# Kernel optimization log

Measured on AMD Instinct MI355X. Metric: run time of the kernel, lower is better.

## Reference

```python
import jax, jax.numpy as jnp
import numpy as np

B, CIN, H, W = 8, 64, 128, 128
COUT, KH, KW = 64, 3, 3
STRIDE, PAD, DIL = 1, 1, 1
HO, WO = 128, 128


def setup_inputs() -> dict:
    key = jax.random.key(0)
    k1, k2, k3 = jax.random.split(key, 3)
    x = jax.random.normal(k1, (B, CIN, H, W), dtype=jnp.float32)
    offset = jax.random.normal(k2, (B, 2 * KH * KW, HO, WO), dtype=jnp.float32)
    fan_in = CIN * KH * KW
    weight = jax.random.normal(k3, (COUT, CIN, KH, KW), dtype=jnp.float32) / np.sqrt(fan_in)
    return {"x": x, "offset": offset, "weight": weight}


def _deform_conv(x, offset, weight):
    b, c, h, w = x.shape
    cout, cin, kh, kw = weight.shape
    k2 = kh * kw
    ho, wo = offset.shape[2], offset.shape[3]
    # offsets: interleaved (dy, dx) per kernel tap
    off = offset.reshape(b, k2, 2, ho, wo)
    dy, dx = off[:, :, 0], off[:, :, 1]                      # [B, K2, Ho, Wo]
    ky = jnp.repeat(jnp.arange(kh), kw).astype(x.dtype)       # [K2]
    kx = jnp.tile(jnp.arange(kw), kh).astype(x.dtype)
    base_y = (jnp.arange(ho) * STRIDE - PAD).astype(x.dtype)  # [Ho]
    base_x = (jnp.arange(wo) * STRIDE - PAD).astype(x.dtype)  # [Wo]
    py = dy + ky[None, :, None, None] * DIL + base_y[None, None, :, None]
    px = dx + kx[None, :, None, None] * DIL + base_x[None, None, None, :]

    y0 = jnp.floor(py)
    x0 = jnp.floor(px)
    wy1 = py - y0
    wx1 = px - x0
    y0i = y0.astype(jnp.int32)
    x0i = x0.astype(jnp.int32)

    def gather_corner(yi, xi, wgt):
        # zero-padding semantics: mask out-of-bounds corners
        valid = ((yi >= 0) & (yi < h) & (xi >= 0) & (xi < w)).astype(x.dtype)
        yc = jnp.clip(yi, 0, h - 1)
        xc = jnp.clip(xi, 0, w - 1)
        def per_batch(xb, yb, xbid, vb, wb):
            return xb[:, yb, xbid] * (vb * wb)[None]          # [C, K2, Ho, Wo]
        return jax.vmap(per_batch)(x, yc, xc, valid, wgt)

    # accumulate 4 corners to avoid holding all gathers at once
    sampled = gather_corner(y0i, x0i, (1 - wy1) * (1 - wx1))
    sampled = sampled + gather_corner(y0i, x0i + 1, (1 - wy1) * wx1)
    sampled = sampled + gather_corner(y0i + 1, x0i, wy1 * (1 - wx1))
    sampled = sampled + gather_corner(y0i + 1, x0i + 1, wy1 * wx1)
    # sampled: [B, Cin, K2, Ho, Wo]; conv-accumulate
    return jnp.einsum('bckhw,ock->bohw', sampled, weight.reshape(cout, cin, k2))


def reference(x, offset, weight):
    return _deform_conv(x, offset, weight)
```

## Files before the change

### kernel.cpp

```cpp
#include <hip/hip_runtime.h>
#include <hip/hip_bf16.h>

#define CIN  64
#define HH   128
#define WW   128
#define COUT 64
#define K2   9
#define HW   (HH * WW)

typedef __attribute__((ext_vector_type(8))) short bf16x8;
typedef __attribute__((ext_vector_type(4))) float f32x4;
typedef __attribute__((ext_vector_type(2))) float f32x2;

__device__ __forceinline__ unsigned short f2bf(float f) {
    __hip_bfloat16 h = __float2bfloat16(f);
    return *reinterpret_cast<unsigned short*>(&h);
}
__device__ __forceinline__ f32x2 up2(unsigned int d) {
    f32x2 r;
    r[0] = __uint_as_float(d << 16);
    r[1] = __uint_as_float(d & 0xffff0000u);
    return r;
}
__device__ __forceinline__ void gl2lds16(const unsigned short* g, unsigned short* l) {
    __builtin_amdgcn_global_load_lds(
        (const __attribute__((address_space(1))) unsigned int*)g,
        (__attribute__((address_space(3))) unsigned int*)l, 16, 0, 0);
}

__launch_bounds__(256)
__global__ void xprep2_kernel(const float* __restrict__ x, unsigned short* __restrict__ xt) {
    const int idx = blockIdx.x * 256 + threadIdx.x;
    const int xw = idx & 127;
    const int y  = (idx >> 7) & 127;
    const int s  = (idx >> 14) & 7;
    const int b  = idx >> 17;
    const float* src = x + (((size_t)(b * CIN + s * 8) * HH) + y) * WW + xw;
    union { unsigned short us[8]; bf16x8 v; } u;
    #pragma unroll
    for (int j = 0; j < 8; ++j) u.us[j] = f2bf(src[(size_t)j * HW]);
    *(bf16x8*)(xt + ((((size_t)b * 8 + s) * HW) + y * WW + xw) * 8) = u.v;
}

__global__ void wprep_kernel(const float* __restrict__ w, unsigned short* __restrict__ wtp) {
    int idx = blockIdx.x * 256 + threadIdx.x;
    if (idx >= COUT * CIN * K2) return;
    int j  = idx & 7;
    int l  = (idx >> 3) & 63;
    int nt = (idx >> 9) & 3;
    int ks = (idx >> 11) & 1;
    int k  = idx >> 12;
    int o  = nt * 16 + (l & 15);
    int c  = ks * 32 + (l >> 4) * 8 + j;
    wtp[idx] = f2bf(w[(o * CIN + c) * K2 + k]);
}

__launch_bounds__(512, 4)
__global__ void dcn_kernel(const unsigned short* __restrict__ xt,
                           const float* __restrict__ off,
                           const unsigned short* __restrict__ wtp,
                           float* __restrict__ out) {
    __shared__ unsigned short lsB[2][4096];
    __shared__ float sred[64][66];

    const int tid = threadIdx.x;
    const int w   = tid >> 6;
    const int l   = tid & 63;
    const int wr  = w & 3;
    const int wh  = w >> 2;

    int bid = blockIdx.x;
    bid = (bid & 7) * 256 + (bid >> 3);
    const int b   = bid >> 8;
    const int t   = bid & 255;
    const int ty0 = (t >> 3) << 2;
    const int tx0 = (t & 7) << 4;

    const int g      = l >> 4;
    const int lane16 = l & 15;

    f32x4 acc[4] = {{0,0,0,0},{0,0,0,0},{0,0,0,0},{0,0,0,0}};

    const float* offb = off + (size_t)b * (2 * K2) * HW;
    const unsigned short* xp = xt + ((size_t)b * 8 + (wh * 4 + g)) * HW * 8;

    const int ypA  = ty0 + wr;
    const int xpA  = tx0 + lane16;
    const int offp = ypA * WW + xpA;

    f32x4 Pw[2];
    int   Pr0[2], Pr1[2];
    float oyv[2], oxv[2];
    bf16x8 Gst[2][4];
    bf16x8 bvv[4];
    bf16x8 af;

#define PARAMS(K, S) do {                                                     \
    const int kdy = (K) / 3 - 1, kdx = (K) % 3 - 1;                           \
    float py = oyv[S] + (float)(ypA + kdy);                                   \
    float px = oxv[S] + (float)(xpA + kdx);                                   \
    float fy = floorf(py), fx = floorf(px);                                   \
    float wy = py - fy, wxn = px - fx;                                        \
    int y0 = (int)fy, x0i = (int)fx;                                          \
    int yc0 = min(max(y0,     0), HH - 1);                                    \
    int yc1 = min(max(y0 + 1, 0), HH - 1);                                    \
    float ay0 = (y0 >= 0  && y0 <= HH - 1) ? (1.f - wy) : 0.f;                \
    float ay1 = (y0 >= -1 && y0 <= HH - 2) ? wy         : 0.f;                \
    int   xL  = min(max(x0i, 0), WW - 2);                                     \
    float bx0 = (x0i >= 0  && x0i <= WW - 1) ? (1.f - wxn) : 0.f;             \
    float bx1 = (x0i >= -1 && x0i <= WW - 2) ? wxn         : 0.f;             \
    bool  sw  = (x0i != xL);                                                  \
    float wxa = sw ? bx1 : bx0;                                               \
    float wxb = sw ? bx0 : bx1;                                               \
    Pw[S][0] = ay0 * wxa; Pw[S][1] = ay0 * wxb;                               \
    Pw[S][2] = ay1 * wxa; Pw[S][3] = ay1 * wxb;                               \
    Pr0[S] = (yc0 * WW + xL) * 8;                                             \
    Pr1[S] = (yc1 * WW + xL) * 8;                                             \
} while (0)

#define GATHER(S) do {                                                        \
    const unsigned short* r0p = xp + Pr0[S];                                  \
    const unsigned short* r1p = xp + Pr1[S];                                  \
    Gst[S][0] = *(const bf16x8*)(r0p); Gst[S][1] = *(const bf16x8*)(r0p + 8); \
    Gst[S][2] = *(const bf16x8*)(r1p); Gst[S][3] = *(const bf16x8*)(r1p + 8); \
} while (0)

#define INTERP(S) do {                                                        \
    union { bf16x8 v; unsigned int d[4]; } ua, ub, uc, ud;                    \
    ua.v = Gst[S][0]; ub.v = Gst[S][1]; uc.v = Gst[S][2]; ud.v = Gst[S][3];   \
    union { unsigned short us[8]; bf16x8 v; } rr;                             \
    _Pragma("unroll")                                                         \
    for (int q = 0; q < 4; ++q) {                                             \
        f32x2 v = up2(ua.d[q]) * Pw[S][0] + up2(ub.d[q]) * Pw[S][1]           \
                + up2(uc.d[q]) * Pw[S][2] + up2(ud.d[q]) * Pw[S][3];          \
        rr.us[2*q]   = f2bf(v[0]);                                            \
        rr.us[2*q+1] = f2bf(v[1]);                                            \
    }                                                                         \
    af = rr.v;                                                                \
} while (0)

#define BVLOAD(P) do {                                                        \
    _Pragma("unroll")                                                         \
    for (int nt = 0; nt < 4; ++nt)                                            \
        bvv[nt] = *(const bf16x8*)(&lsB[P][(wh * 4 + nt) * 512 + l * 8]);     \
} while (0)

#define STAGE(P, K) do {                                                      \
    gl2lds16(wtp + (K) * 4096 + w * 512 + l * 8, &lsB[P][w * 512]);           \
} while (0)

#define DOMFMA() do {                                                         \
    __builtin_amdgcn_s_setprio(1);                                            \
    _Pragma("unroll")                                                         \
    for (int nt = 0; nt < 4; ++nt)                                            \
        acc[nt] = __builtin_amdgcn_mfma_f32_16x16x32_bf16(af, bvv[nt], acc[nt], 0, 0, 0); \
    __builtin_amdgcn_s_setprio(0);                                            \
} while (0)

    STAGE(0, 0);
    oyv[0] = offb[offp];          oxv[0] = offb[HW + offp];
    oyv[1] = offb[2 * HW + offp]; oxv[1] = offb[3 * HW + offp];
    PARAMS(0, 0);
    GATHER(0);
    __syncthreads();

    #pragma unroll
    for (int s = 0; s < K2; ++s) {
        const int cur = s & 1, nxt = cur ^ 1;
        if (s < 8) {
            STAGE(nxt, s + 1);
            PARAMS(s + 1, nxt);
            if (s < 7) {
                oyv[cur] = offb[(2 * (s + 2)    ) * HW + offp];
                oxv[cur] = offb[(2 * (s + 2) + 1) * HW + offp];
            }
            GATHER(nxt);
        }
        BVLOAD(cur);
        INTERP(cur);
        DOMFMA();
        if (s < 8) __syncthreads();
    }

#undef PARAMS
#undef GATHER
#undef INTERP
#undef BVLOAD
#undef STAGE
#undef DOMFMA

    const int rq = g * 4;
    if (wh == 0) {
        #pragma unroll
        for (int nt = 0; nt < 4; ++nt)
            #pragma unroll
            for (int j = 0; j < 4; ++j)
                sred[wr * 16 + rq + j][nt * 16 + lane16] = acc[nt][j];
    }
    __syncthreads();
    if (wh == 1) {
        #pragma unroll
        for (int nt = 0; nt < 4; ++nt) {
            f32x4 v;
            #pragma unroll
            for (int j = 0; j < 4; ++j)
                v[j] = sred[wr * 16 + rq + j][nt * 16 + lane16] + acc[nt][j];
            const int o  = nt * 16 + lane16;
            const int yy = ty0 + wr;
            const int xx = tx0 + rq;
            *(f32x4*)&out[(((size_t)b * COUT + o) * HH + yy) * WW + xx] = v;
        }
    }
}

__global__ void wprep_fb(const float* __restrict__ w, unsigned short* __restrict__ wt) {
    int idx = blockIdx.x * 256 + threadIdx.x;
    if (idx >= COUT * CIN * K2) return;
    int o = idx / (CIN * K2);
    int r = idx % (CIN * K2);
    int k = r / CIN;
    int c = r % CIN;
    wt[idx] = f2bf(w[o * (CIN * K2) + c * K2 + k]);
}

__launch_bounds__(256)
__global__ void dcn_fb(const float* __restrict__ x, const float* __restrict__ off,
                       const unsigned short* __restrict__ wt, float* __restrict__ out) {
    __shared__ unsigned short s_s[64 * 66];
    const int tid = threadIdx.x;
    const int w = tid >> 6, l = tid & 63;
    const int bid = blockIdx.x;
    const int b = bid >> 8, t = bid & 255;
    const int ty0 = (t >> 4) << 3, tx0 = (t & 15) << 3;
    const int iy = l >> 3, ix = l & 7;
    const int ypix = ty0 + iy, xpix = tx0 + ix;
    f32x4 acc[4] = {{0,0,0,0},{0,0,0,0},{0,0,0,0},{0,0,0,0}};
    const int c0w = w * 16;
    for (int k = 0; k < K2; ++k) {
        float dy = off[(((b * (2*K2)) + 2*k    ) * HH + ypix) * WW + xpix];
        float dx = off[(((b * (2*K2)) + 2*k + 1) * HH + ypix) * WW + xpix];
        float py = dy + (float)(k / 3 + ypix - 1);
        float px = dx + (float)(k % 3 + xpix - 1);
        float fy = floorf(py), fx = floorf(px);
        float wy = py - fy, wx = px - fx;
        int y0 = (int)fy, x0 = (int)fx;
        int yc0 = min(max(y0, 0), HH-1), yc1 = min(max(y0+1, 0), HH-1);
        float ay0 = (y0 >= 0 && y0 <= HH-1) ? (1.f-wy) : 0.f;
        float ay1 = (y0 >= -1 && y0 <= HH-2) ? wy : 0.f;
        int xL = min(max(x0, 0), WW-2);
        float bx0 = (x0 >= 0 && x0 <= WW-1) ? (1.f-wx) : 0.f;
        float bx1 = (x0 >= -1 && x0 <= WW-2) ? wx : 0.f;
        bool sw = (x0 != xL);
        float wxa = sw ? bx1 : bx0, wxb = sw ? bx0 : bx1;
        float W0x = ay0*wxa, W0y = ay0*wxb, W1x = ay1*wxa, W1y = ay1*wxb;
        const float* r0 = x + ((b * CIN + c0w) * HH + yc0) * WW + xL;
        const float* r1 = x + ((b * CIN + c0w) * HH + yc1) * WW + xL;
        unsigned short* sd = &s_s[l * 66 + c0w];
        #pragma unroll
        for (int cc = 0; cc < 16; ++cc) {
            sd[cc] = f2bf(W0x*r0[0] + W0y*r0[1] + W1x*r1[0] + W1y*r1[1]);
            r0 += HH*WW; r1 += HH*WW;
        }
        __syncthreads();
        const int o_lane = l & 15, q = l >> 4;
        #pragma unroll
        for (int ks = 0; ks < 2; ++ks) {
            const int cb = ks*32 + q*8;
            const int row = w*16 + o_lane;
            const unsigned int* sp = (const unsigned int*)s_s;
            const int ib = row*33 + (cb >> 1);
            union { unsigned int u[4]; bf16x8 v; } af;
            af.u[0]=sp[ib]; af.u[1]=sp[ib+1]; af.u[2]=sp[ib+2]; af.u[3]=sp[ib+3];
            #pragma unroll
            for (int nt = 0; nt < 4; ++nt) {
                bf16x8 bfv = *(const bf16x8*)(wt + (nt*16 + o_lane) * (CIN*K2) + k*64 + cb);
                acc[nt] = __builtin_amdgcn_mfma_f32_16x16x32_bf16(af.v, bfv, acc[nt], 0, 0, 0);
            }
        }
        __syncthreads();
    }
    const int o_lane = l & 15, rq = (l >> 4) * 4;
    #pragma unroll
    for (int nt = 0; nt < 4; ++nt) {
        const int o = nt*16 + o_lane;
        #pragma unroll
        for (int j = 0; j < 4; ++j) {
            const int pix = w*16 + rq + j;
            out[(((size_t)b * COUT + o) * HH + ty0 + (pix>>3)) * WW + tx0 + (pix&7)] = acc[nt][j];
        }
    }
}

extern "C" void kernel_launch(void* const* d_in, const int* in_sizes, int n_in,
                              void* d_out, int out_size, void* d_ws, size_t ws_size,
                              hipStream_t stream) {
    const float* x   = (const float*)d_in[0];
    const float* off = (const float*)d_in[1];
    const float* wgt = (const float*)d_in[2];
    float* out = (float*)d_out;

    const size_t xt_bytes = (size_t)8 * HW * 64 * sizeof(unsigned short);
    const size_t wt_bytes = (size_t)COUT * CIN * K2 * sizeof(unsigned short);

    if (ws_size >= xt_bytes + wt_bytes) {
        unsigned short* xt  = (unsigned short*)d_ws;
        unsigned short* wtp = (unsigned short*)((char*)d_ws + xt_bytes);
        xprep2_kernel<<<4096, 256, 0, stream>>>(x, xt);
        wprep_kernel<<<(COUT * CIN * K2 + 255) / 256, 256, 0, stream>>>(wgt, wtp);
        dcn_kernel<<<2048, 512, 0, stream>>>(xt, off, wtp, out);
    } else {
        unsigned short* wt = (unsigned short*)d_ws;
        wprep_fb<<<(COUT * CIN * K2 + 255) / 256, 256, 0, stream>>>(wgt, wt);
        dcn_fb<<<2048, 256, 0, stream>>>(x, off, wt, out);
    }
}
```

Measured before the change: 62.20 us.

## Preload all weight taps into LDS once and drop per-tap barriers

Weights for all nine kernel taps are now loaded into dynamic shared memory once at kernel start, replacing the per-tap double-buffered staging. This removes the per-iteration __syncthreads and the interleaved global-to-LDS copies from the main loop. The reduction buffer is aliased onto the same shared memory after a barrier. The cost is a 72 KB LDS footprint per block, which may cut the number of resident blocks per CU and raise the up-front load latency.

Measured after the change: 57.34 us. 7.8% less time.

```diff
diff --git a/kernel.cpp b/kernel.cpp
--- a/kernel.cpp
+++ b/kernel.cpp
@@ -60,9 +60,7 @@
                            const float* __restrict__ off,
                            const unsigned short* __restrict__ wtp,
                            float* __restrict__ out) {
-    __shared__ unsigned short lsB[2][4096];
-    __shared__ float sred[64][66];
-
+    extern __shared__ unsigned short lsB[];
     const int tid = threadIdx.x;
     const int w   = tid >> 6;
     const int l   = tid & 63;
@@ -78,6 +76,12 @@
 
     const int g      = l >> 4;
     const int lane16 = l & 15;
+
+    #pragma unroll
+    for (int r = 0; r < 9; ++r) {
+        const int seg = r * 8 + w;
+        gl2lds16(wtp + seg * 512 + l * 8, lsB + seg * 512);
+    }
 
     f32x4 acc[4] = {{0,0,0,0},{0,0,0,0},{0,0,0,0},{0,0,0,0}};
 
@@ -139,25 +143,21 @@
     af = rr.v;                                                                \
 } while (0)
 
-#define BVLOAD(P) do {                                                        \
+#define BVLOAD(K) do {                                                        \
     _Pragma("unroll")                                                         \
     for (int nt = 0; nt < 4; ++nt)                                            \
-        bvv[nt] = *(const bf16x8*)(&lsB[P][(wh * 4 + nt) * 512 + l * 8]);     \
-} while (0)
-
-#define STAGE(P, K) do {                                                      \
-    gl2lds16(wtp + (K) * 4096 + w * 512 + l * 8, &lsB[P][w * 512]);           \
+        bvv[nt] = *(const bf16x8*)(&lsB[(((K) * 2 + wh) * 4 + nt) * 512 + l * 8]); \
 } while (0)
 
 #define DOMFMA() do {                                                         \
     __builtin_amdgcn_s_setprio(1);                                            \
-    _Pragma("unroll")                                                         \
-    for (int nt = 0; nt < 4; ++nt)                                            \
-        acc[nt] = __builtin_amdgcn_mfma_f32_16x16x32_bf16(af, bvv[nt], acc[nt], 0, 0, 0); \
+    acc[0] = __builtin_amdgcn_mfma_f32_16x16x32_bf16(af, bvv[0], acc[0], 0, 0, 0); \
+    acc[1] = __builtin_amdgcn_mfma_f32_16x16x32_bf16(af, bvv[1], acc[1], 0, 0, 0); \
+    acc[2] = __builtin_amdgcn_mfma_f32_16x16x32_bf16(af, bvv[2], acc[2], 0, 0, 0); \
+    acc[3] = __builtin_amdgcn_mfma_f32_16x16x32_bf16(af, bvv[3], acc[3], 0, 0, 0); \
     __builtin_amdgcn_s_setprio(0);                                            \
 } while (0)
 
-    STAGE(0, 0);
     oyv[0] = offb[offp];          oxv[0] = offb[HW + offp];
     oyv[1] = offb[2 * HW + offp]; oxv[1] = offb[3 * HW + offp];
     PARAMS(0, 0);
@@ -168,7 +168,6 @@
     for (int s = 0; s < K2; ++s) {
         const int cur = s & 1, nxt = cur ^ 1;
         if (s < 8) {
-            STAGE(nxt, s + 1);
             PARAMS(s + 1, nxt);
             if (s < 7) {
                 oyv[cur] = offb[(2 * (s + 2)    ) * HW + offp];
@@ -176,19 +175,19 @@
             }
             GATHER(nxt);
         }
-        BVLOAD(cur);
+        BVLOAD(s);
         INTERP(cur);
         DOMFMA();
-        if (s < 8) __syncthreads();
     }
 
 #undef PARAMS
 #undef GATHER
 #undef INTERP
 #undef BVLOAD
-#undef STAGE
 #undef DOMFMA
 
+    float (*sred)[66] = (float (*)[66])lsB;
+    __syncthreads();
     const int rq = g * 4;
     if (wh == 0) {
         #pragma unroll
@@ -307,7 +306,7 @@
         unsigned short* wtp = (unsigned short*)((char*)d_ws + xt_bytes);
         xprep2_kernel<<<4096, 256, 0, stream>>>(x, xt);
         wprep_kernel<<<(COUT * CIN * K2 + 255) / 256, 256, 0, stream>>>(wgt, wtp);
-        dcn_kernel<<<2048, 512, 0, stream>>>(xt, off, wtp, out);
+        dcn_kernel<<<2048, 512, 73728, stream>>>(xt, off, wtp, out);
     } else {
         unsigned short* wt = (unsigned short*)d_ws;
         wprep_fb<<<(COUT * CIN * K2 + 255) / 256, 256, 0, stream>>>(wgt, wt);
```
